# Kernel optimization log

Hardware: AMD Instinct MI355X
Metric: run time of the kernel (lower is better)

Reference implementation:

```python
import jax, jax.numpy as jnp
import numpy as np

N = 50000   # nodes
E = 800000  # edges (before self-loops)
DIN = 128
H, C = 4, 32
HC = H * C  # 128
DE = 3      # edge feature dim
G = 64      # graphs in batch
HID = 32
DOUT = 1
LN_EPS = 1e-5


def setup_inputs() -> dict:
    key = jax.random.key(0)
    ks = iter(jax.random.split(key, 64))
    def nrm(shape, s=0.1):
        return jax.random.normal(next(ks), shape, dtype=jnp.float32) * s
    inp = {}
    inp["x"] = jax.random.normal(next(ks), (N, DIN), dtype=jnp.float32)
    inp["edge_index"] = jax.random.randint(next(ks), (2, E), 0, N, dtype=jnp.int32)
    inp["batch"] = jnp.sort(jax.random.randint(next(ks), (N,), 0, G, dtype=jnp.int32))
    inp["edge_attr"] = jax.random.normal(next(ks), (E, DE), dtype=jnp.float32)
    # GATv2 layers: layer0 in=DIN(128); layers 1,2 in=HC(128)
    for l, din in enumerate([DIN, HC, HC]):
        inp[f"Wl{l}"] = nrm((HC, din)); inp[f"bl{l}"] = jnp.zeros((HC,), jnp.float32)
        inp[f"Wr{l}"] = nrm((HC, din)); inp[f"br{l}"] = jnp.zeros((HC,), jnp.float32)
        inp[f"We{l}"] = nrm((HC, DE))
        inp[f"att{l}"] = nrm((H, C))
        inp[f"bo{l}"] = jnp.zeros((HC,), jnp.float32)
    for l in range(2):
        inp[f"ln{l}_g"] = jnp.ones((HC,), jnp.float32)
        inp[f"ln{l}_b"] = jnp.zeros((HC,), jnp.float32)
    # post-processing MLP: 128->32->32->32->1
    inp["pw1"] = nrm((HID, HC)); inp["pb1"] = jnp.zeros((HID,), jnp.float32)
    inp["pw2"] = nrm((HID, HID)); inp["pb2"] = jnp.zeros((HID,), jnp.float32)
    inp["pw3"] = nrm((HID, HID)); inp["pb3"] = jnp.zeros((HID,), jnp.float32)
    inp["pw4"] = nrm((DOUT, HID)); inp["pb4"] = jnp.zeros((DOUT,), jnp.float32)
    return inp


def _gat_layer(x, src, dst, eattr, Wl, bl, Wr, br, We, att, bo):
    # GATv2Conv (concat heads). x_l from lin_l -> source, x_r from lin_r -> target.
    xl = (x @ Wl.T + bl).reshape(-1, H, C)
    xr = (x @ Wr.T + br).reshape(-1, H, C)
    e = (eattr @ We.T).reshape(-1, H, C)
    m = jax.nn.leaky_relu(xl[src] + xr[dst] + e, negative_slope=0.2)  # [E',H,C]
    s = jnp.einsum('ehc,hc->eh', m, att)                              # [E',H]
    smax = jax.ops.segment_max(s, dst, num_segments=N)
    ex = jnp.exp(s - smax[dst])
    den = jax.ops.segment_sum(ex, dst, num_segments=N)
    alpha = ex / (den[dst] + 1e-16)
    out = jax.ops.segment_sum(alpha[:, :, None] * xl[src], dst, num_segments=N)
    return out.reshape(-1, HC) + bo


def _ln(x, g, b):
    mu = jnp.mean(x, axis=-1, keepdims=True)
    var = jnp.mean((x - mu) ** 2, axis=-1, keepdims=True)
    return (x - mu) * jax.lax.rsqrt(var + LN_EPS) * g + b


def _forward(x, edge_attr, edge_index, batch, p):
    src0, dst0 = edge_index[0], edge_index[1]
    # PyG add_self_loops with fill_value='mean': per-dst-node mean of edge_attr
    cnt = jax.ops.segment_sum(jnp.ones((E,), jnp.float32), dst0, num_segments=N)
    loop_attr = jax.ops.segment_sum(edge_attr, dst0, num_segments=N) / jnp.maximum(cnt, 1.0)[:, None]
    ar = jnp.arange(N, dtype=src0.dtype)
    src = jnp.concatenate([src0, ar]); dst = jnp.concatenate([dst0, ar])
    ea = jnp.concatenate([edge_attr, loop_attr], axis=0)
    embedding = x
    for l in range(3):
        x = _gat_layer(x, src, dst, ea, p[f"Wl{l}"], p[f"bl{l}"], p[f"Wr{l}"],
                       p[f"br{l}"], p[f"We{l}"], p[f"att{l}"], p[f"bo{l}"])
        embedding = x
        x = jax.nn.relu(x)  # dropout inactive (eval)
        if l != 2:
            x = _ln(x, p[f"ln{l}_g"], p[f"ln{l}_b"])
    pooled = jax.ops.segment_max(x, batch, num_segments=G)
    pooled = jnp.where(jnp.isfinite(pooled), pooled, 0.0)
    h = jax.nn.relu(pooled @ p["pw1"].T + p["pb1"])
    h = jax.nn.relu(h @ p["pw2"].T + p["pb2"])
    h = jax.nn.relu(h @ p["pw3"].T + p["pb3"])
    out = h @ p["pw4"].T + p["pb4"]
    return embedding, out


def reference(x, edge_index, batch, edge_attr,
              Wl0, bl0, Wr0, br0, We0, att0, bo0,
              Wl1, bl1, Wr1, br1, We1, att1, bo1,
              Wl2, bl2, Wr2, br2, We2, att2, bo2,
              ln0_g, ln0_b, ln1_g, ln1_b,
              pw1, pb1, pw2, pb2, pw3, pb3, pw4, pb4):
    p = dict(Wl0=Wl0, bl0=bl0, Wr0=Wr0, br0=br0, We0=We0, att0=att0, bo0=bo0,
             Wl1=Wl1, bl1=bl1, Wr1=Wr1, br1=br1, We1=We1, att1=att1, bo1=bo1,
             Wl2=Wl2, bl2=bl2, Wr2=Wr2, br2=br2, We2=We2, att2=att2, bo2=bo2,
             ln0_g=ln0_g, ln0_b=ln0_b, ln1_g=ln1_g, ln1_b=ln1_b,
             pw1=pw1, pb1=pb1, pw2=pw2, pb2=pb2, pw3=pw3, pb3=pb3, pw4=pw4, pb4=pb4)
    return _forward(x, edge_attr, edge_index, batch, p)
```

## Files before the change

### kernel.cpp

```cpp
#include <hip/hip_runtime.h>
#include <math.h>


#define LN_EPS 1e-5f
#define LOG2E 1.44269504088896340736f
#define CHUNK 4096
#define BCAP 8192

typedef short bf16x8 __attribute__((ext_vector_type(8)));
typedef float f32x4 __attribute__((ext_vector_type(4)));
typedef float f32x2 __attribute__((ext_vector_type(2)));

static __device__ __forceinline__ unsigned short f2bf(float f) {
  unsigned int u = __float_as_uint(f);
  u += 0x7fffu + ((u >> 16) & 1u);
  return (unsigned short)(u >> 16);
}

static __device__ __forceinline__ float dpp_sum8(float v) {
  int x;
  x = __builtin_amdgcn_update_dpp(0, __float_as_int(v), 0x0B1, 0xf, 0xf, true);
  v += __int_as_float(x);
  x = __builtin_amdgcn_update_dpp(0, __float_as_int(v), 0x04E, 0xf, 0xf, true);
  v += __int_as_float(x);
  x = __builtin_amdgcn_update_dpp(0, __float_as_int(v), 0x141, 0xf, 0xf, true);
  v += __int_as_float(x);
  return v;
}


__global__ __launch_bounds__(256) void k_pre(
    const int* __restrict__ ei, const float* __restrict__ ea,
    int* __restrict__ gcnt, float4* __restrict__ staged, int E, int nbuk, int nbinA,
    const float* __restrict__ w0, const float* __restrict__ w1,
    const float* __restrict__ w2, const float* __restrict__ w3,
    const float* __restrict__ w4, const float* __restrict__ w5,
    unsigned short* __restrict__ Wb,
    const float* __restrict__ We0, const float* __restrict__ att0,
    const float* __restrict__ We1, const float* __restrict__ att1,
    const float* __restrict__ We2, const float* __restrict__ att2,
    float* __restrict__ tab) {
  __shared__ int hist[256];
  __shared__ int basebuf[256];
  int b = blockIdx.x;
  int t = threadIdx.x;

  if (b < nbinA) {
    int e0 = b * CHUNK;
    hist[t] = 0;
    __syncthreads();
#pragma unroll
    for (int i = 0; i < CHUNK / 256; ++i) {
      int e = e0 + i * 256 + t;
      if (e < E) atomicAdd(&hist[ei[E + e] >> 8], 1);
    }
    __syncthreads();
    int h = hist[t];
    if (t < nbuk && h > 0) basebuf[t] = t * BCAP + atomicAdd(&gcnt[t], h);
    hist[t] = 0;
    __syncthreads();
#pragma unroll
    for (int i = 0; i < CHUNK / 256; ++i) {
      int e = e0 + i * 256 + t;
      if (e < E) {
        int s = ei[e];
        int d = ei[E + e];
        int bk = d >> 8;
        int r = atomicAdd(&hist[bk], 1);
        float4 rec;
        rec.x = ea[e * 3 + 0];
        rec.y = ea[e * 3 + 1];
        rec.z = ea[e * 3 + 2];
        rec.w = __int_as_float(s | (d << 16));
        staged[basebuf[bk] + r] = rec;
      }
    }
  } else if (b < nbinA + 384) {
    int bb = b - nbinA;
    const float* srcs[6] = {w0, w1, w2, w3, w4, w5};
    int mtx = bb >> 6;
    int i = (bb & 63) * 256 + t;
    Wb[(size_t)mtx * 16384 + i] = f2bf(srcs[mtx][i]);
  } else {
    if (t < 96) {
      int l = t >> 5;
      int sl = t & 31;
      const float* We = (l == 0) ? We0 : ((l == 1) ? We1 : We2);
      const float* att = (l == 0) ? att0 : ((l == 1) ? att1 : att2);
      float* o = tab + (size_t)l * 512 + sl * 16;
#pragma unroll
      for (int j = 0; j < 4; ++j) {
        o[j] = We[(sl * 4 + j) * 3 + 0];
        o[4 + j] = We[(sl * 4 + j) * 3 + 1];
        o[8 + j] = We[(sl * 4 + j) * 3 + 2];
        o[12 + j] = att[sl * 4 + j] * LOG2E;
      }
    }
  }
}

__global__ void k_bscan(const int* __restrict__ gcnt, int* __restrict__ bukStart,
                        int* __restrict__ offs, float4* __restrict__ e4,
                        int N, int nbuk, int EP) {
  __shared__ int sh[256];
  int t = threadIdx.x;
  int nodes = (t < nbuk) ? min(256, N - t * 256) : 0;
  int v = (t < nbuk) ? gcnt[t] + nodes : 0;
  sh[t] = v;
  __syncthreads();
  for (int d = 1; d < 256; d <<= 1) {
    int add = (t >= d) ? sh[t - d] : 0;
    __syncthreads();
    sh[t] += add;
    __syncthreads();
  }
  if (t < nbuk) bukStart[t] = sh[t] - v;
  if (t == 0) offs[N] = EP;
  if (t < 8) {
    float4 r;
    r.x = 0.f; r.y = 0.f; r.z = 0.f;
    r.w = __int_as_float(0);
    e4[EP + t] = r;
  }
}

__global__ __launch_bounds__(256) void k_binB(const float4* __restrict__ staged,
                                              const int* __restrict__ gcnt,
                                              const int* __restrict__ bukStart,
                                              float4* __restrict__ e4,
                                              int* __restrict__ offs, int N) {
  __shared__ int hist[256], cur[256], begS[256], sh[256];
  int t = threadIdx.x;
  int b = blockIdx.x;
  int n0 = b * 256;
  int nn = min(256, N - n0);
  int m = gcnt[b];
  size_t sbase = (size_t)b * BCAP;

  hist[t] = 0;
  __syncthreads();
  for (int p = t; p < m; p += 256) {
    unsigned int u = (unsigned int)__float_as_int(staged[sbase + p].w);
    atomicAdd(&hist[(int)(u >> 16) - n0], 1);
  }
  __syncthreads();
  int v = (t < nn) ? hist[t] + 1 : 0;
  sh[t] = v;
  __syncthreads();
  for (int d = 1; d < 256; d <<= 1) {
    int add = (t >= d) ? sh[t - d] : 0;
    __syncthreads();
    sh[t] += add;
    __syncthreads();
  }
  if (t < nn) {
    int base = bukStart[b] + sh[t] - v;
    cur[t] = base;
    begS[t] = base;
    offs[n0 + t] = base;
  }
  __syncthreads();
  for (int p = t; p < m; p += 256) {
    float4 rec = staged[sbase + p];
    unsigned int u = (unsigned int)__float_as_int(rec.w);
    int pos = atomicAdd(&cur[(int)(u >> 16) - n0], 1);
    rec.w = __int_as_float((int)(u & 0xffffu) * 256);
    e4[pos] = rec;
  }
  __syncthreads();
  if (t < nn) {
    int beg = begS[t], last = cur[t];
    float s0 = 0.f, s1 = 0.f, s2 = 0.f;
    for (int p = beg; p < last; ++p) {
      float4 r = e4[p];
      s0 += r.x;
      s1 += r.y;
      s2 += r.z;
    }
    float invc = 1.0f / fmaxf((float)(last - beg), 1.0f);
    float4 r;
    r.x = s0 * invc;
    r.y = s1 * invc;
    r.z = s2 * invc;
    r.w = __int_as_float((n0 + t) * 256);
    e4[last] = r;
  }
}

template <bool F32IN>
__global__ __launch_bounds__(256) void k_gemm_fused(const float* __restrict__ xf,
                                                    const unsigned short* __restrict__ xb,
                                                    const unsigned short* __restrict__ Wb,
                                                    const float* __restrict__ bl,
                                                    const float* __restrict__ br,
                                                    unsigned short* __restrict__ xlb,
                                                    unsigned short* __restrict__ xrb, int N) {
  int wave = threadIdx.x >> 6;
  int lane = threadIdx.x & 63;
  const unsigned short* WL = Wb;
  const unsigned short* WR = Wb + 16384;

  int row0 = (blockIdx.x * 4 + wave) * 16;
  if (row0 >= N) return;
  int m = lane & 15;
  int q = lane >> 4;

  int brow = row0 + m;
  if (brow >= N) brow = N - 1;

  bf16x8 bfrag[4];
  if constexpr (F32IN) {
    const float* xrow = xf + (size_t)brow * 128 + q * 8;
#pragma unroll
    for (int kt = 0; kt < 4; ++kt) {
      float4 u0 = *(const float4*)(xrow + kt * 32);
      float4 u1 = *(const float4*)(xrow + kt * 32 + 4);
      bf16x8 f;
      f[0] = (short)f2bf(u0.x); f[1] = (short)f2bf(u0.y);
      f[2] = (short)f2bf(u0.z); f[3] = (short)f2bf(u0.w);
      f[4] = (short)f2bf(u1.x); f[5] = (short)f2bf(u1.y);
      f[6] = (short)f2bf(u1.z); f[7] = (short)f2bf(u1.w);
      bfrag[kt] = f;
    }
  } else {
    const unsigned short* xrow = xb + (size_t)brow * 128 + q * 8;
#pragma unroll
    for (int kt = 0; kt < 4; ++kt) bfrag[kt] = *(const bf16x8*)(xrow + kt * 32);
  }

  f32x4 accL[8], accR[8];
#pragma unroll
  for (int jt = 0; jt < 8; ++jt) {
    accL[jt] = (f32x4){0.f, 0.f, 0.f, 0.f};
    accR[jt] = (f32x4){0.f, 0.f, 0.f, 0.f};
  }

  const unsigned short* wl = WL + (size_t)m * 128 + q * 8;
  const unsigned short* wr = WR + (size_t)m * 128 + q * 8;
#pragma unroll
  for (int kt = 0; kt < 4; ++kt) {
#pragma unroll
    for (int jt = 0; jt < 8; ++jt) {
      bf16x8 aL = *(const bf16x8*)(wl + (size_t)jt * 2048 + kt * 32);
      accL[jt] = __builtin_amdgcn_mfma_f32_16x16x32_bf16(aL, bfrag[kt], accL[jt], 0, 0, 0);
      bf16x8 aR = *(const bf16x8*)(wr + (size_t)jt * 2048 + kt * 32);
      accR[jt] = __builtin_amdgcn_mfma_f32_16x16x32_bf16(aR, bfrag[kt], accR[jt], 0, 0, 0);
    }
  }

  int node = row0 + m;
  if (node < N) {
    unsigned short* ol = xlb + (size_t)node * 128 + q * 4;
    unsigned short* orr = xrb + (size_t)node * 128 + q * 4;
#pragma unroll
    for (int jt = 0; jt < 8; ++jt) {
      float4 bsL = *(const float4*)&bl[jt * 16 + q * 4];
      uint2 pL;
      pL.x = (unsigned int)f2bf(accL[jt][0] + bsL.x) | ((unsigned int)f2bf(accL[jt][1] + bsL.y) << 16);
      pL.y = (unsigned int)f2bf(accL[jt][2] + bsL.z) | ((unsigned int)f2bf(accL[jt][3] + bsL.w) << 16);
      *(uint2*)(ol + jt * 16) = pL;
      float4 bsR = *(const float4*)&br[jt * 16 + q * 4];
      uint2 pR;
      pR.x = (unsigned int)f2bf(accR[jt][0] + bsR.x) | ((unsigned int)f2bf(accR[jt][1] + bsR.y) << 16);
      pR.y = (unsigned int)f2bf(accR[jt][2] + bsR.z) | ((unsigned int)f2bf(accR[jt][3] + bsR.w) << 16);
      *(uint2*)(orr + jt * 16) = pR;
    }
  }
}

__global__ __launch_bounds__(256) void k_agg(const unsigned short* __restrict__ xlb,
                                             const unsigned short* __restrict__ xrb,
                                             const float4* __restrict__ e4,
                                             const int* __restrict__ offs,
                                             const float* __restrict__ scoreTab,
                                             const float* __restrict__ bo,
                                             const float* __restrict__ lng, const float* __restrict__ lnb,
                                             unsigned short* __restrict__ xnext_bf,
                                             float* __restrict__ emb, int last, int N) {
  int w = (blockIdx.x * blockDim.x + threadIdx.x) >> 6;
  if (w >= N) return;
  int lane = threadIdx.x & 63;
  int half = lane >> 5;
  int sl = lane & 31;
  int c = sl * 4;
  unsigned int c2 = (unsigned int)(c * 2);
  int beg = offs[w], end = offs[w + 1];
  int cnt = end - beg;

  f32x2 xr01, xr23, wea01, wea23, web01, web23, wec01, wec23, at01, at23;
  {
    const float4* tp = (const float4*)(scoreTab + (size_t)sl * 16);
    float4 pa = tp[0], pb = tp[1], pc = tp[2], pt = tp[3];
    wea01[0] = pa.x; wea01[1] = pa.y; wea23[0] = pa.z; wea23[1] = pa.w;
    web01[0] = pb.x; web01[1] = pb.y; web23[0] = pb.z; web23[1] = pb.w;
    wec01[0] = pc.x; wec01[1] = pc.y; wec23[0] = pc.z; wec23[1] = pc.w;
    at01[0] = pt.x; at01[1] = pt.y; at23[0] = pt.z; at23[1] = pt.w;
    uint2 vr = *(const uint2*)&xrb[(size_t)w * 128 + c];
    xr01[0] = __uint_as_float(vr.x << 16);
    xr01[1] = __uint_as_float(vr.x & 0xffff0000u);
    xr23[0] = __uint_as_float(vr.y << 16);
    xr23[1] = __uint_as_float(vr.y & 0xffff0000u);
  }

  const char* e4B = (const char*)e4;
  const char* xlB = (const char*)xlb;

  float l = 0.f;
  f32x2 acc01 = {0.f, 0.f}, acc23 = {0.f, 0.f};

  unsigned int lastoff = (unsigned int)(end - 1) << 4;
  int T = (cnt + 1) >> 1;

  unsigned int o0 = (unsigned int)(beg + half) << 4;
  if (o0 > lastoff) o0 = lastoff;
  unsigned int o1 = o0 + 32u;
  if (o1 > lastoff) o1 = lastoff;
  unsigned int o2 = o1 + 32u;
  if (o2 > lastoff) o2 = lastoff;
  float4 e0 = *(const float4*)(e4B + o0);
  float4 e1 = *(const float4*)(e4B + o1);
  float4 e2 = *(const float4*)(e4B + o2);
  uint2 g0 = *(const uint2*)(xlB + ((unsigned int)__float_as_int(e0.w) + c2));
  uint2 g1 = *(const uint2*)(xlB + ((unsigned int)__float_as_int(e1.w) + c2));
  unsigned int offP = o2;

  auto compute = [&](const float4& e, uint2 v, bool valid) {
    f32x2 xl01, xl23;
    xl01[0] = __uint_as_float(v.x << 16);
    xl01[1] = __uint_as_float(v.x & 0xffff0000u);
    xl23[0] = __uint_as_float(v.y << 16);
    xl23[1] = __uint_as_float(v.y & 0xffff0000u);
    f32x2 ex = {e.x, e.x}, ey = {e.y, e.y}, ez = {e.z, e.z};
    f32x2 t01 = __builtin_elementwise_fma(wea01, ex,
                  __builtin_elementwise_fma(web01, ey,
                    __builtin_elementwise_fma(wec01, ez, xr01 + xl01)));
    f32x2 t23 = __builtin_elementwise_fma(wea23, ex,
                  __builtin_elementwise_fma(web23, ey,
                    __builtin_elementwise_fma(wec23, ez, xr23 + xl23)));
    t01 = __builtin_elementwise_max(t01, t01 * 0.2f);
    t23 = __builtin_elementwise_max(t23, t23 * 0.2f);
    f32x2 d2 = __builtin_elementwise_fma(t01, at01, t23 * at23);
    float s = d2[0] + d2[1];
    float wgt = __builtin_amdgcn_exp2f(dpp_sum8(s));
    if (!valid) wgt = 0.f;
    l += wgt;
    f32x2 w2 = {wgt, wgt};
    acc01 = __builtin_elementwise_fma(xl01, w2, acc01);
    acc23 = __builtin_elementwise_fma(xl23, w2, acc23);
  };

#pragma unroll 2
  for (int it = 0; it < T - 3; ++it) {
    unsigned int o3 = offP + 32u;
    if (o3 > lastoff) o3 = lastoff;
    float4 e3 = *(const float4*)(e4B + o3);
    uint2 g2 = *(const uint2*)(xlB + ((unsigned int)__float_as_int(e2.w) + c2));
    compute(e0, g0, true);
    e0 = e1; e1 = e2; e2 = e3;
    g0 = g1; g1 = g2;
    offP = o3;
  }
  if (T >= 3) {
    uint2 g2 = *(const uint2*)(xlB + ((unsigned int)__float_as_int(e2.w) + c2));
    compute(e0, g0, true);
    e0 = e1; e1 = e2;
    g0 = g1; g1 = g2;
  }
  if (T >= 2) {
    compute(e0, g0, true);
    e0 = e1;
    g0 = g1;
  }
  {
    int idx = 2 * (T - 1) + half;
    compute(e0, g0, idx < cnt);
  }

  l += __shfl_xor(l, 32);
  float a0 = acc01[0]; a0 += __shfl_xor(a0, 32);
  float a1 = acc01[1]; a1 += __shfl_xor(a1, 32);
  float a2 = acc23[0]; a2 += __shfl_xor(a2, 32);
  float a3 = acc23[1]; a3 += __shfl_xor(a3, 32);

  float inv = 1.0f / l;
  f32x4 o4;
  const float4 bo4 = *(const float4*)&bo[c];
  o4[0] = a0 * inv + bo4.x;
  o4[1] = a1 * inv + bo4.y;
  o4[2] = a2 * inv + bo4.z;
  o4[3] = a3 * inv + bo4.w;

  if (last) {
    if (half == 0) {
      float4 st = {o4[0], o4[1], o4[2], o4[3]};
      *(float4*)&emb[(size_t)w * 128 + c] = st;
    }
  } else {
    f32x4 r;
    r[0] = fmaxf(o4[0], 0.f);
    r[1] = fmaxf(o4[1], 0.f);
    r[2] = fmaxf(o4[2], 0.f);
    r[3] = fmaxf(o4[3], 0.f);
    float s = r[0] + r[1] + r[2] + r[3];
    s += __shfl_xor(s, 1);
    s += __shfl_xor(s, 2);
    s += __shfl_xor(s, 4);
    s += __shfl_xor(s, 8);
    s += __shfl_xor(s, 16);
    float mu = s * 0.0078125f;
    f32x4 d;
    d[0] = r[0] - mu;
    d[1] = r[1] - mu;
    d[2] = r[2] - mu;
    d[3] = r[3] - mu;
    float v2 = d[0] * d[0] + d[1] * d[1] + d[2] * d[2] + d[3] * d[3];
    v2 += __shfl_xor(v2, 1);
    v2 += __shfl_xor(v2, 2);
    v2 += __shfl_xor(v2, 4);
    v2 += __shfl_xor(v2, 8);
    v2 += __shfl_xor(v2, 16);
    float var = v2 * 0.0078125f;
    float rstd = rsqrtf(var + LN_EPS);
    if (half == 0) {
      const float4 g4 = *(const float4*)&lng[c];
      const float4 b4 = *(const float4*)&lnb[c];
      float o0 = d[0] * rstd * g4.x + b4.x;
      float o1 = d[1] * rstd * g4.y + b4.y;
      float o2 = d[2] * rstd * g4.z + b4.z;
      float o3 = d[3] * rstd * g4.w + b4.w;
      uint2 pack;
      pack.x = (unsigned int)f2bf(o0) | ((unsigned int)f2bf(o1) << 16);
      pack.y = (unsigned int)f2bf(o2) | ((unsigned int)f2bf(o3) << 16);
      *(uint2*)&xnext_bf[(size_t)w * 128 + c] = pack;
    }
  }
}

__global__ void k_pool(const float* __restrict__ emb, const int* __restrict__ batch,
                       float* __restrict__ pooled, int N) {
  int c = threadIdx.x & 127;
  int half = threadIdx.x >> 7;
  int base = blockIdx.x * 64 + half;
  int limit = min(blockIdx.x * 64 + 64, N);
  float cur = 0.f;
  int curg = -1;
  for (int n = base; n < limit; n += 2) {
    int g = batch[n];
    if (g != curg) {
      if (curg >= 0) atomicMax((unsigned int*)&pooled[curg * 128 + c], __float_as_uint(cur));
      curg = g;
      cur = 0.f;
    }
    cur = fmaxf(cur, emb[(size_t)n * 128 + c]);
  }
  if (curg >= 0) atomicMax((unsigned int*)&pooled[curg * 128 + c], __float_as_uint(cur));
}

__global__ void k_mlp(const float* __restrict__ pooled,
                      const float* __restrict__ pw1, const float* __restrict__ pb1,
                      const float* __restrict__ pw2, const float* __restrict__ pb2,
                      const float* __restrict__ pw3, const float* __restrict__ pb3,
                      const float* __restrict__ pw4, const float* __restrict__ pb4,
                      float* __restrict__ out) {
  int g = blockIdx.x;
  int t = threadIdx.x;
  __shared__ float buf1[32], buf2[32];
  if (t < 32) {
    float acc = pb1[t];
    for (int k = 0; k < 128; ++k) acc += pw1[t * 128 + k] * pooled[g * 128 + k];
    buf1[t] = fmaxf(acc, 0.f);
  }
  __syncthreads();
  if (t < 32) {
    float acc = pb2[t];
    for (int k = 0; k < 32; ++k) acc += pw2[t * 32 + k] * buf1[k];
    buf2[t] = fmaxf(acc, 0.f);
  }
  __syncthreads();
  if (t < 32) {
    float acc = pb3[t];
    for (int k = 0; k < 32; ++k) acc += pw3[t * 32 + k] * buf2[k];
    buf1[t] = fmaxf(acc, 0.f);
  }
  __syncthreads();
  if (t == 0) {
    float acc = pb4[0];
    for (int k = 0; k < 32; ++k) acc += pw4[k] * buf1[k];
    out[g] = acc;
  }
}


extern "C" void kernel_launch(void* const* d_in, const int* in_sizes, int n_in,
                              void* d_out, int out_size, void* d_ws, size_t ws_size,
                              hipStream_t stream) {
  const float* x_in = (const float*)d_in[0];
  const int* ei = (const int*)d_in[1];
  const int* batch = (const int*)d_in[2];
  const float* ea = (const float*)d_in[3];

  const int N = in_sizes[0] / 128;
  const int E = in_sizes[1] / 2;
  const int EP = E + N;
  const int G = out_size - N * 128;
  const int NBUK = (N + 255) / 256;
  const int NBINA = (E + CHUNK - 1) / CHUNK;

  const float *Wl[3], *bl[3], *Wr[3], *br[3], *We[3], *att[3], *bo[3];
  for (int l = 0; l < 3; ++l) {
    Wl[l] = (const float*)d_in[4 + 7 * l];
    bl[l] = (const float*)d_in[5 + 7 * l];
    Wr[l] = (const float*)d_in[6 + 7 * l];
    br[l] = (const float*)d_in[7 + 7 * l];
    We[l] = (const float*)d_in[8 + 7 * l];
    att[l] = (const float*)d_in[9 + 7 * l];
    bo[l] = (const float*)d_in[10 + 7 * l];
  }
  const float* lng[2] = {(const float*)d_in[25], (const float*)d_in[27]};
  const float* lnb[2] = {(const float*)d_in[26], (const float*)d_in[28]};
  const float* pw1 = (const float*)d_in[29];
  const float* pb1 = (const float*)d_in[30];
  const float* pw2 = (const float*)d_in[31];
  const float* pb2 = (const float*)d_in[32];
  const float* pw3 = (const float*)d_in[33];
  const float* pb3 = (const float*)d_in[34];
  const float* pw4 = (const float*)d_in[35];
  const float* pb4 = (const float*)d_in[36];

  char* base = (char*)d_ws;
  size_t cur = 0;
  auto carve = [&](size_t bytes) -> char* {
    char* p = base + cur;
    cur += (bytes + 255) & ~(size_t)255;
    return p;
  };
  unsigned short* xlb = (unsigned short*)carve((size_t)N * 128 * 2);
  unsigned short* xrb = (unsigned short*)carve((size_t)N * 128 * 2);
  unsigned short* xb = (unsigned short*)carve((size_t)N * 128 * 2);
  unsigned short* Wb = (unsigned short*)carve((size_t)6 * 16384 * 2);
  float4* e4 = (float4*)carve((size_t)(EP + 8) * 16);
  float4* staged = (float4*)carve((size_t)NBUK * BCAP * 16);
  int* offs = (int*)carve((size_t)(N + 1) * 4);
  int* gcnt = (int*)carve((size_t)NBUK * 4);
  int* bukStart = (int*)carve((size_t)(NBUK + 1) * 4);
  float* scoreTab = (float*)carve((size_t)3 * 512 * 4);
  float* pooled = (float*)carve((size_t)G * 128 * 4);

  float* emb_out = (float*)d_out;
  float* mlp_out = (float*)d_out + (size_t)N * 128;

  hipMemsetAsync(gcnt, 0, (size_t)NBUK * 4, stream);
  hipMemsetAsync(pooled, 0, (size_t)G * 128 * 4, stream);

  k_pre<<<NBINA + 384 + 1, 256, 0, stream>>>(ei, ea, gcnt, staged, E, NBUK, NBINA,
                                             Wl[0], Wr[0], Wl[1], Wr[1], Wl[2], Wr[2], Wb,
                                             We[0], att[0], We[1], att[1], We[2], att[2],
                                             scoreTab);
  k_bscan<<<1, 256, 0, stream>>>(gcnt, bukStart, offs, e4, N, NBUK, EP);
  k_binB<<<NBUK, 256, 0, stream>>>(staged, gcnt, bukStart, e4, offs, N);

  for (int l = 0; l < 3; ++l) {
    dim3 ggrid((N + 63) / 64);
    if (l == 0) {
      k_gemm_fused<true><<<ggrid, 256, 0, stream>>>(x_in, xb, Wb, bl[0], br[0], xlb, xrb, N);
    } else {
      k_gemm_fused<false><<<ggrid, 256, 0, stream>>>(nullptr, xb, Wb + (size_t)l * 32768,
                                                     bl[l], br[l], xlb, xrb, N);
    }
    int last = (l == 2) ? 1 : 0;
    const float* g = last ? bo[l] : lng[l];
    const float* b = last ? bo[l] : lnb[l];
    k_agg<<<(N * 64 + 255) / 256, 256, 0, stream>>>(xlb, xrb, e4, offs,
                                                    scoreTab + (size_t)l * 512,
                                                    bo[l], g, b,
                                                    xb, emb_out, last, N);
  }

  k_pool<<<(N + 63) / 64, 256, 0, stream>>>(emb_out, batch, pooled, N);
  k_mlp<<<G, 64, 0, stream>>>(pooled, pw1, pb1, pw2, pb2, pw3, pb3, pw4, pb4, mlp_out);
}
```

Before: 505.8 us.

## Pre-pack GEMM operands in MFMA fragment order and fuse bucket scan into binning

Weights are converted into an MFMA-fragment-ordered bf16 layout, and the aggregation kernel writes the next layer's activations directly in that packed layout, so GEMM loads become contiguous per-lane vector loads. GEMM outputs are staged through LDS so each wave writes full contiguous rows. The separate bucket-scan kernel is folded into each binning block, which redundantly recomputes the prefix, and per-node edge-attribute means are accumulated with LDS atomics instead of a serial re-read loop. The main risks are the redundant scan work in every block and contention on the float LDS atomics.

```diff
diff --git a/kernel.cpp b/kernel.cpp
--- a/kernel.cpp
+++ b/kernel.cpp
@@ -27,7 +27,6 @@
   v += __int_as_float(x);
   return v;
 }
-
 
 __global__ __launch_bounds__(256) void k_pre(
     const int* __restrict__ ei, const float* __restrict__ ea,
@@ -75,12 +74,18 @@
         staged[basebuf[bk] + r] = rec;
       }
     }
-  } else if (b < nbinA + 384) {
+  } else if (b < nbinA + 48) {
     int bb = b - nbinA;
     const float* srcs[6] = {w0, w1, w2, w3, w4, w5};
-    int mtx = bb >> 6;
-    int i = (bb & 63) * 256 + t;
-    Wb[(size_t)mtx * 16384 + i] = f2bf(srcs[mtx][i]);
+    int mtx = bb >> 3;
+    int c = (bb & 7) * 256 + t;
+    int lane = c & 63;
+    int kt = (c >> 6) & 3;
+    int jt = c >> 8;
+    const float* s = srcs[mtx] + (size_t)(jt * 16 + (lane & 15)) * 128 + kt * 32 + (lane >> 4) * 8;
+    unsigned short* d = Wb + (size_t)mtx * 16384 + (size_t)c * 8;
+#pragma unroll
+    for (int j = 0; j < 8; ++j) d[j] = f2bf(s[j]);
   } else {
     if (t < 96) {
       int l = t >> 5;
@@ -99,37 +104,12 @@
   }
 }
 
-__global__ void k_bscan(const int* __restrict__ gcnt, int* __restrict__ bukStart,
-                        int* __restrict__ offs, float4* __restrict__ e4,
-                        int N, int nbuk, int EP) {
-  __shared__ int sh[256];
-  int t = threadIdx.x;
-  int nodes = (t < nbuk) ? min(256, N - t * 256) : 0;
-  int v = (t < nbuk) ? gcnt[t] + nodes : 0;
-  sh[t] = v;
-  __syncthreads();
-  for (int d = 1; d < 256; d <<= 1) {
-    int add = (t >= d) ? sh[t - d] : 0;
-    __syncthreads();
-    sh[t] += add;
-    __syncthreads();
-  }
-  if (t < nbuk) bukStart[t] = sh[t] - v;
-  if (t == 0) offs[N] = EP;
-  if (t < 8) {
-    float4 r;
-    r.x = 0.f; r.y = 0.f; r.z = 0.f;
-    r.w = __int_as_float(0);
-    e4[EP + t] = r;
-  }
-}
-
 __global__ __launch_bounds__(256) void k_binB(const float4* __restrict__ staged,
                                               const int* __restrict__ gcnt,
-                                              const int* __restrict__ bukStart,
                                               float4* __restrict__ e4,
-                                              int* __restrict__ offs, int N) {
+                                              int* __restrict__ offs, int N, int nbuk, int EP) {
   __shared__ int hist[256], cur[256], begS[256], sh[256];
+  __shared__ float sX[256], sY[256], sZ[256];
   int t = threadIdx.x;
   int b = blockIdx.x;
   int n0 = b * 256;
@@ -137,7 +117,32 @@
   int m = gcnt[b];
   size_t sbase = (size_t)b * BCAP;
 
+  {
+    int nodes_t = (t < nbuk) ? min(256, N - t * 256) : 0;
+    int v0 = (t < nbuk) ? gcnt[t] + nodes_t : 0;
+    sh[t] = v0;
+    __syncthreads();
+    for (int d = 1; d < 256; d <<= 1) {
+      int add = (t >= d) ? sh[t - d] : 0;
+      __syncthreads();
+      sh[t] += add;
+      __syncthreads();
+    }
+  }
+  int bukStart_b = (b == 0) ? 0 : sh[b - 1];
+  if (b == 0) {
+    if (t == 0) offs[N] = EP;
+    if (t < 8) {
+      float4 r;
+      r.x = 0.f; r.y = 0.f; r.z = 0.f;
+      r.w = __int_as_float(0);
+      e4[EP + t] = r;
+    }
+  }
+  __syncthreads();
+
   hist[t] = 0;
+  sX[t] = 0.f; sY[t] = 0.f; sZ[t] = 0.f;
   __syncthreads();
   for (int p = t; p < m; p += 256) {
     unsigned int u = (unsigned int)__float_as_int(staged[sbase + p].w);
@@ -154,7 +159,7 @@
     __syncthreads();
   }
   if (t < nn) {
-    int base = bukStart[b] + sh[t] - v;
+    int base = bukStart_b + sh[t] - v;
     cur[t] = base;
     begS[t] = base;
     offs[n0 + t] = base;
@@ -163,25 +168,22 @@
   for (int p = t; p < m; p += 256) {
     float4 rec = staged[sbase + p];
     unsigned int u = (unsigned int)__float_as_int(rec.w);
-    int pos = atomicAdd(&cur[(int)(u >> 16) - n0], 1);
+    int d = (int)(u >> 16) - n0;
+    int pos = atomicAdd(&cur[d], 1);
+    atomicAdd(&sX[d], rec.x);
+    atomicAdd(&sY[d], rec.y);
+    atomicAdd(&sZ[d], rec.z);
     rec.w = __int_as_float((int)(u & 0xffffu) * 256);
     e4[pos] = rec;
   }
   __syncthreads();
   if (t < nn) {
     int beg = begS[t], last = cur[t];
-    float s0 = 0.f, s1 = 0.f, s2 = 0.f;
-    for (int p = beg; p < last; ++p) {
-      float4 r = e4[p];
-      s0 += r.x;
-      s1 += r.y;
-      s2 += r.z;
-    }
     float invc = 1.0f / fmaxf((float)(last - beg), 1.0f);
     float4 r;
-    r.x = s0 * invc;
-    r.y = s1 * invc;
-    r.z = s2 * invc;
+    r.x = sX[t] * invc;
+    r.y = sY[t] * invc;
+    r.z = sZ[t] * invc;
     r.w = __int_as_float((n0 + t) * 256);
     e4[last] = r;
   }
@@ -189,12 +191,13 @@
 
 template <bool F32IN>
 __global__ __launch_bounds__(256) void k_gemm_fused(const float* __restrict__ xf,
-                                                    const unsigned short* __restrict__ xb,
+                                                    const unsigned short* __restrict__ xpack,
                                                     const unsigned short* __restrict__ Wb,
                                                     const float* __restrict__ bl,
                                                     const float* __restrict__ br,
                                                     unsigned short* __restrict__ xlb,
                                                     unsigned short* __restrict__ xrb, int N) {
+  __shared__ unsigned short sld[4][2048];
   int wave = threadIdx.x >> 6;
   int lane = threadIdx.x & 63;
   const unsigned short* WL = Wb;
@@ -205,11 +208,10 @@
   int m = lane & 15;
   int q = lane >> 4;
 
-  int brow = row0 + m;
-  if (brow >= N) brow = N - 1;
-
   bf16x8 bfrag[4];
   if constexpr (F32IN) {
+    int brow = row0 + m;
+    if (brow >= N) brow = N - 1;
     const float* xrow = xf + (size_t)brow * 128 + q * 8;
 #pragma unroll
     for (int kt = 0; kt < 4; ++kt) {
@@ -223,9 +225,9 @@
       bfrag[kt] = f;
     }
   } else {
-    const unsigned short* xrow = xb + (size_t)brow * 128 + q * 8;
-#pragma unroll
-    for (int kt = 0; kt < 4; ++kt) bfrag[kt] = *(const bf16x8*)(xrow + kt * 32);
+    const unsigned short* xrow = xpack + (size_t)(row0 >> 4) * 2048 + lane * 8;
+#pragma unroll
+    for (int kt = 0; kt < 4; ++kt) bfrag[kt] = *(const bf16x8*)(xrow + kt * 512);
   }
 
   f32x4 accL[8], accR[8];
@@ -235,36 +237,44 @@
     accR[jt] = (f32x4){0.f, 0.f, 0.f, 0.f};
   }
 
-  const unsigned short* wl = WL + (size_t)m * 128 + q * 8;
-  const unsigned short* wr = WR + (size_t)m * 128 + q * 8;
 #pragma unroll
   for (int kt = 0; kt < 4; ++kt) {
 #pragma unroll
     for (int jt = 0; jt < 8; ++jt) {
-      bf16x8 aL = *(const bf16x8*)(wl + (size_t)jt * 2048 + kt * 32);
+      bf16x8 aL = *(const bf16x8*)(WL + (size_t)(jt * 4 + kt) * 512 + lane * 8);
       accL[jt] = __builtin_amdgcn_mfma_f32_16x16x32_bf16(aL, bfrag[kt], accL[jt], 0, 0, 0);
-      bf16x8 aR = *(const bf16x8*)(wr + (size_t)jt * 2048 + kt * 32);
+      bf16x8 aR = *(const bf16x8*)(WR + (size_t)(jt * 4 + kt) * 512 + lane * 8);
       accR[jt] = __builtin_amdgcn_mfma_f32_16x16x32_bf16(aR, bfrag[kt], accR[jt], 0, 0, 0);
     }
   }
 
-  int node = row0 + m;
-  if (node < N) {
-    unsigned short* ol = xlb + (size_t)node * 128 + q * 4;
-    unsigned short* orr = xrb + (size_t)node * 128 + q * 4;
-#pragma unroll
-    for (int jt = 0; jt < 8; ++jt) {
-      float4 bsL = *(const float4*)&bl[jt * 16 + q * 4];
-      uint2 pL;
-      pL.x = (unsigned int)f2bf(accL[jt][0] + bsL.x) | ((unsigned int)f2bf(accL[jt][1] + bsL.y) << 16);
-      pL.y = (unsigned int)f2bf(accL[jt][2] + bsL.z) | ((unsigned int)f2bf(accL[jt][3] + bsL.w) << 16);
-      *(uint2*)(ol + jt * 16) = pL;
-      float4 bsR = *(const float4*)&br[jt * 16 + q * 4];
-      uint2 pR;
-      pR.x = (unsigned int)f2bf(accR[jt][0] + bsR.x) | ((unsigned int)f2bf(accR[jt][1] + bsR.y) << 16);
-      pR.y = (unsigned int)f2bf(accR[jt][2] + bsR.z) | ((unsigned int)f2bf(accR[jt][3] + bsR.w) << 16);
-      *(uint2*)(orr + jt * 16) = pR;
-    }
+#pragma unroll
+  for (int jt = 0; jt < 8; ++jt) {
+    float4 bs = *(const float4*)&bl[jt * 16 + q * 4];
+    uint2 p;
+    p.x = (unsigned int)f2bf(accL[jt][0] + bs.x) | ((unsigned int)f2bf(accL[jt][1] + bs.y) << 16);
+    p.y = (unsigned int)f2bf(accL[jt][2] + bs.z) | ((unsigned int)f2bf(accL[jt][3] + bs.w) << 16);
+    *(uint2*)&sld[wave][m * 128 + jt * 16 + q * 4] = p;
+  }
+#pragma unroll
+  for (int r = 0; r < 4; ++r) {
+    uint4 vv = *(const uint4*)&sld[wave][r * 512 + lane * 8];
+    int node = row0 + r * 4 + (lane >> 4);
+    if (node < N) *(uint4*)(xlb + (size_t)row0 * 128 + r * 512 + lane * 8) = vv;
+  }
+#pragma unroll
+  for (int jt = 0; jt < 8; ++jt) {
+    float4 bs = *(const float4*)&br[jt * 16 + q * 4];
+    uint2 p;
+    p.x = (unsigned int)f2bf(accR[jt][0] + bs.x) | ((unsigned int)f2bf(accR[jt][1] + bs.y) << 16);
+    p.y = (unsigned int)f2bf(accR[jt][2] + bs.z) | ((unsigned int)f2bf(accR[jt][3] + bs.w) << 16);
+    *(uint2*)&sld[wave][m * 128 + jt * 16 + q * 4] = p;
+  }
+#pragma unroll
+  for (int r = 0; r < 4; ++r) {
+    uint4 vv = *(const uint4*)&sld[wave][r * 512 + lane * 8];
+    int node = row0 + r * 4 + (lane >> 4);
+    if (node < N) *(uint4*)(xrb + (size_t)row0 * 128 + r * 512 + lane * 8) = vv;
   }
 }
 
@@ -275,7 +285,7 @@
                                              const float* __restrict__ scoreTab,
                                              const float* __restrict__ bo,
                                              const float* __restrict__ lng, const float* __restrict__ lnb,
-                                             unsigned short* __restrict__ xnext_bf,
+                                             unsigned short* __restrict__ xnext_pack,
                                              float* __restrict__ emb, int last, int N) {
   int w = (blockIdx.x * blockDim.x + threadIdx.x) >> 6;
   if (w >= N) return;
@@ -431,7 +441,10 @@
       uint2 pack;
       pack.x = (unsigned int)f2bf(o0) | ((unsigned int)f2bf(o1) << 16);
       pack.y = (unsigned int)f2bf(o2) | ((unsigned int)f2bf(o3) << 16);
-      *(uint2*)&xnext_bf[(size_t)w * 128 + c] = pack;
+      int kt = sl >> 3;
+      int qq = (sl >> 1) & 3;
+      size_t elem = (size_t)(w >> 4) * 2048 + kt * 512 + (qq * 16 + (w & 15)) * 8 + (sl & 1) * 4;
+      *(uint2*)&xnext_pack[elem] = pack;
     }
   }
 }
@@ -536,13 +549,12 @@
   };
   unsigned short* xlb = (unsigned short*)carve((size_t)N * 128 * 2);
   unsigned short* xrb = (unsigned short*)carve((size_t)N * 128 * 2);
-  unsigned short* xb = (unsigned short*)carve((size_t)N * 128 * 2);
+  unsigned short* xpack = (unsigned short*)carve(((size_t)((N + 15) / 16) + 1) * 2048 * 2);
   unsigned short* Wb = (unsigned short*)carve((size_t)6 * 16384 * 2);
   float4* e4 = (float4*)carve((size_t)(EP + 8) * 16);
   float4* staged = (float4*)carve((size_t)NBUK * BCAP * 16);
   int* offs = (int*)carve((size_t)(N + 1) * 4);
   int* gcnt = (int*)carve((size_t)NBUK * 4);
-  int* bukStart = (int*)carve((size_t)(NBUK + 1) * 4);
   float* scoreTab = (float*)carve((size_t)3 * 512 * 4);
   float* pooled = (float*)carve((size_t)G * 128 * 4);
 
@@ -552,19 +564,18 @@
   hipMemsetAsync(gcnt, 0, (size_t)NBUK * 4, stream);
   hipMemsetAsync(pooled, 0, (size_t)G * 128 * 4, stream);
 
-  k_pre<<<NBINA + 384 + 1, 256, 0, stream>>>(ei, ea, gcnt, staged, E, NBUK, NBINA,
-                                             Wl[0], Wr[0], Wl[1], Wr[1], Wl[2], Wr[2], Wb,
-                                             We[0], att[0], We[1], att[1], We[2], att[2],
-                                             scoreTab);
-  k_bscan<<<1, 256, 0, stream>>>(gcnt, bukStart, offs, e4, N, NBUK, EP);
-  k_binB<<<NBUK, 256, 0, stream>>>(staged, gcnt, bukStart, e4, offs, N);
+  k_pre<<<NBINA + 48 + 1, 256, 0, stream>>>(ei, ea, gcnt, staged, E, NBUK, NBINA,
+                                            Wl[0], Wr[0], Wl[1], Wr[1], Wl[2], Wr[2], Wb,
+                                            We[0], att[0], We[1], att[1], We[2], att[2],
+                                            scoreTab);
+  k_binB<<<NBUK, 256, 0, stream>>>(staged, gcnt, e4, offs, N, NBUK, EP);
 
   for (int l = 0; l < 3; ++l) {
     dim3 ggrid((N + 63) / 64);
     if (l == 0) {
-      k_gemm_fused<true><<<ggrid, 256, 0, stream>>>(x_in, xb, Wb, bl[0], br[0], xlb, xrb, N);
+      k_gemm_fused<true><<<ggrid, 256, 0, stream>>>(x_in, xpack, Wb, bl[0], br[0], xlb, xrb, N);
     } else {
-      k_gemm_fused<false><<<ggrid, 256, 0, stream>>>(nullptr, xb, Wb + (size_t)l * 32768,
+      k_gemm_fused<false><<<ggrid, 256, 0, stream>>>(nullptr, xpack, Wb + (size_t)l * 32768,
                                                      bl[l], br[l], xlb, xrb, N);
     }
     int last = (l == 2) ? 1 : 0;
@@ -573,7 +584,7 @@
     k_agg<<<(N * 64 + 255) / 256, 256, 0, stream>>>(xlb, xrb, e4, offs,
                                                     scoreTab + (size_t)l * 512,
                                                     bo[l], g, b,
-                                                    xb, emb_out, last, N);
+                                                    xpack, emb_out, last, N);
   }
 
   k_pool<<<(N + 63) / 64, 256, 0, stream>>>(emb_out, batch, pooled, N);
```

After: 470.8 us. 6.9% less time.
